# Kernel tuning notes

Measured on AMD Instinct MI355X. Metric: run time of the kernel, lower is better.

Reference implementation:

```python
import jax, jax.numpy as jnp
import numpy as np
from jax import lax

NSITE, NCELL, BSZ = 101, 64, 1
D_MODEL, D_INNER, D_STATE, D_CONV, DT_RANK = 64, 128, 16, 4, 4
L = NSITE * NCELL


def setup_inputs() -> dict:
    key = jax.random.key(0)
    ks = jax.random.split(key, 16)
    f = lambda k, s, sc=0.05: jax.random.normal(k, s, jnp.float32) * sc
    return {
        "DNAinput": f(ks[0], (BSZ, L, 32), 1.0),
        "CpGinput": f(ks[1], (BSZ, L, 16), 1.0),
        "cellinput": f(ks[2], (BSZ, L, 16), 1.0),
        "pos": f(ks[3], (BSZ, L, D_MODEL), 1.0),
        "y_true": jax.random.uniform(ks[4], (64,), jnp.float32),
        "W_fcc": f(ks[5], (64, D_MODEL)),
        "b_fcc": jnp.zeros((D_MODEL,), jnp.float32),
        "W_in": f(ks[6], (D_MODEL, 2 * D_INNER)),
        "conv_w": f(ks[7], (D_INNER, D_CONV)),
        "conv_b": jnp.zeros((D_INNER,), jnp.float32),
        "W_xp": f(ks[8], (D_INNER, DT_RANK + 2 * D_STATE)),
        "W_dt": f(ks[9], (DT_RANK, D_INNER)),
        "b_dt": f(ks[10], (D_INNER,)),
        "A_log": jnp.log(jnp.broadcast_to(jnp.arange(1, D_STATE + 1, dtype=jnp.float32), (D_INNER, D_STATE))),
        "Dres": jnp.ones((D_INNER,), jnp.float32),
        "W_out": f(ks[11], (D_INNER, D_MODEL)),
        "ln_g": jnp.ones((D_MODEL,), jnp.float32),
        "ln_b": jnp.zeros((D_MODEL,), jnp.float32),
        "W_fc": f(ks[12], (D_MODEL, 1)),
        "b_fc": jnp.zeros((1,), jnp.float32),
        "halfwin": 50,
        "row_index_s": jax.random.randint(ks[13], (64,), 0, NCELL),
    }


def _silu(x):
    return x * jax.nn.sigmoid(x)


def _layernorm(x, g, b, eps=1e-5):
    m = jnp.mean(x, -1, keepdims=True)
    v = jnp.var(x, -1, keepdims=True)
    return (x - m) * lax.rsqrt(v + eps) * g + b


def _mamba(x, W_in, conv_w, conv_b, W_xp, W_dt, b_dt, A_log, Dres, W_out):
    # x: (B, L, d_model)
    xz = x @ W_in                                   # (B, L, 2*d_inner)
    xi, z = jnp.split(xz, 2, axis=-1)
    # depthwise causal conv1d, kernel D_CONV
    xt = xi.transpose(0, 2, 1)                      # (B, d_inner, L)
    xc = lax.conv_general_dilated(
        xt, conv_w[:, None, :], (1,), [(D_CONV - 1, 0)],
        feature_group_count=D_INNER, dimension_numbers=("NCH", "OIH", "NCH"))
    xc = _silu((xc + conv_b[None, :, None]).transpose(0, 2, 1))  # (B, L, d_inner)
    xdbl = xc @ W_xp                                # (B, L, dt_rank + 2*d_state)
    dt = jax.nn.softplus(xdbl[..., :DT_RANK] @ W_dt + b_dt)      # (B, L, d_inner)
    Bm = xdbl[..., DT_RANK:DT_RANK + D_STATE]       # (B, L, d_state)
    Cm = xdbl[..., DT_RANK + D_STATE:]              # (B, L, d_state)
    A = -jnp.exp(A_log)                             # (d_inner, d_state)
    a_bar = jnp.exp(dt[..., None] * A)              # (B, L, d_inner, d_state)
    b_bar = (dt * xc)[..., None] * Bm[..., None, :]

    def comb(e1, e2):
        a1, b1 = e1
        a2, b2 = e2
        return a1 * a2, a2 * b1 + b2

    _, h = lax.associative_scan(comb, (a_bar, b_bar), axis=1)    # h_t = a_t h_{t-1} + b_t
    y = jnp.einsum("blds,bls->bld", h, Cm) + xc * Dres
    return (y * _silu(z)) @ W_out


def reference(DNAinput, CpGinput, cellinput, pos, y_true, W_fcc, b_fcc, W_in, conv_w, conv_b, W_xp, W_dt, b_dt, A_log, Dres, W_out, ln_g, ln_b, W_fc, b_fc, halfwin, row_index_s):
    x = jnp.concatenate((CpGinput, cellinput, DNAinput), -1) + pos
    x = (x @ W_fcc + b_fcc).reshape(BSZ, -1, D_MODEL)
    mb = lambda u: _mamba(u, W_in, conv_w, conv_b, W_xp, W_dt, b_dt, A_log, Dres, W_out)
    for _ in range(4):
        x = _layernorm(x + (mb(x) + jnp.flip(mb(jnp.flip(x, 1)), 1)) / 2, ln_g, ln_b)
        x = x.reshape(BSZ, NSITE, NCELL, D_MODEL).transpose(0, 2, 1, 3).reshape(BSZ, -1, D_MODEL)
        x = _layernorm(x + (mb(x) + jnp.flip(mb(jnp.flip(x, 1)), 1)) / 2, ln_g, ln_b)
        x = x.reshape(BSZ, NCELL, NSITE, D_MODEL).transpose(0, 2, 1, 3).reshape(BSZ, -1, D_MODEL)
    y_hat = (x.reshape(BSZ, NSITE, NCELL, D_MODEL) @ W_fc + b_fc)[..., 0]  # (B, nsite, ncell)
    y_sel = y_hat[0, halfwin, row_index_s].reshape(-1)
    return 1.0 - jnp.abs(y_true - jax.nn.sigmoid(y_sel))
```

## Files before the change

### kernel.cpp

```cpp
#include <hip/hip_runtime.h>
#include <math.h>

#define L_SEQ 6464
#define DM 64
#define DI 128
#define DS 16
#define CHUNK 101
#define NCH 64

__global__ void k_embed(const float* __restrict__ DNA, const float* __restrict__ CpG,
                        const float* __restrict__ cell, const float* __restrict__ pos,
                        const float* __restrict__ Wfcc, const float* __restrict__ bfcc,
                        float* __restrict__ x0) {
    int l = blockIdx.x;
    int j = threadIdx.x;
    __shared__ float in64[64];
    float v;
    if (j < 16)       v = CpG[l * 16 + j];
    else if (j < 32)  v = cell[l * 16 + (j - 16)];
    else              v = DNA[l * 32 + (j - 32)];
    v += pos[l * 64 + j];
    in64[j] = v;
    __syncthreads();
    float acc = bfcc[j];
    for (int i = 0; i < 64; i++) acc += in64[i] * Wfcc[i * 64 + j];
    x0[(size_t)l * 64 + j] = acc;
}

__global__ void __launch_bounds__(256) k_gemm_in(const float* __restrict__ x,
                                                 const float* __restrict__ Win,
                                                 float* __restrict__ xz) {
    __shared__ float s_x[8][64];
    int t0 = blockIdx.x * 8;
    int tid = threadIdx.x;
    for (int i = tid; i < 8 * 64; i += 256) {
        int rr = i >> 6, c = i & 63;
        s_x[rr][c] = x[(size_t)(t0 + rr) * 64 + c];
    }
    __syncthreads();
    int j = tid;
    float acc[8];
    #pragma unroll
    for (int r = 0; r < 8; r++) acc[r] = 0.f;
    for (int i = 0; i < 64; i++) {
        float w = Win[i * 256 + j];
        #pragma unroll
        for (int r = 0; r < 8; r++) acc[r] = fmaf(s_x[r][i], w, acc[r]);
    }
    #pragma unroll
    for (int r = 0; r < 8; r++) xz[(size_t)(t0 + r) * 256 + j] = acc[r];
}

__global__ void __launch_bounds__(256) k_convdt(
        const float* __restrict__ xz, const float* __restrict__ convw,
        const float* __restrict__ convb, const float* __restrict__ Wxp,
        const float* __restrict__ Wdt, const float* __restrict__ bdt,
        float* __restrict__ xc, float* __restrict__ dt, float* __restrict__ BC) {
    __shared__ __align__(16) float s_xi[22][128];
    __shared__ __align__(16) float s_xc[16][128];
    __shared__ float s_xd[16][36];
    __shared__ __align__(16) float s_wxpT[36][132];
    int t0 = blockIdx.x * 16;
    int tid = threadIdx.x;
    for (int i = tid; i < 36 * 128; i += 256) {
        int ii = i / 36, t = i - ii * 36;
        s_wxpT[t][ii] = Wxp[i];
    }
    for (int i = tid; i < 22 * 32; i += 256) {
        int rr = i >> 5, q = i & 31;
        int r = t0 - 3 + rr;
        float4 v = make_float4(0.f, 0.f, 0.f, 0.f);
        if (r >= 0 && r < L_SEQ) v = *(const float4*)&xz[(size_t)r * 256 + 4 * q];
        s_xi[rr][4 * q + 0] = v.x;
        s_xi[rr][4 * q + 1] = v.y;
        s_xi[rr][4 * q + 2] = v.z;
        s_xi[rr][4 * q + 3] = v.w;
    }
    __syncthreads();
    for (int dir = 0; dir < 2; dir++) {
        for (int i = tid; i < 16 * 128; i += 256) {
            int rr = i >> 7, d = i & 127;
            int lr = rr + 3;
            float acc = convb[d];
            if (dir == 0) {
                #pragma unroll
                for (int k = 0; k < 4; k++) acc += convw[d * 4 + k] * s_xi[lr - 3 + k][d];
            } else {
                #pragma unroll
                for (int k = 0; k < 4; k++) acc += convw[d * 4 + k] * s_xi[lr + 3 - k][d];
            }
            float v = acc / (1.f + expf(-acc));
            s_xc[rr][d] = v;
            xc[((size_t)dir * L_SEQ + t0 + rr) * 128 + d] = v;
        }
        __syncthreads();
        for (int o = tid; o < 16 * 36; o += 256) {
            int rr = o / 36, t = o % 36;
            float acc = 0.f;
            #pragma unroll 8
            for (int i = 0; i < 128; i += 4) {
                const float4 xv = *(const float4*)&s_xc[rr][i];
                const float4 wv = *(const float4*)&s_wxpT[t][i];
                acc = fmaf(xv.x, wv.x, acc);
                acc = fmaf(xv.y, wv.y, acc);
                acc = fmaf(xv.z, wv.z, acc);
                acc = fmaf(xv.w, wv.w, acc);
            }
            s_xd[rr][t] = acc;
        }
        __syncthreads();
        for (int o = tid; o < 16 * 128; o += 256) {
            int rr = o >> 7, d = o & 127;
            float pre = bdt[d];
            #pragma unroll
            for (int r = 0; r < 4; r++) pre += s_xd[rr][r] * Wdt[r * 128 + d];
            float dtv = (pre > 20.f) ? pre : log1pf(expf(pre));
            dt[((size_t)dir * L_SEQ + t0 + rr) * 128 + d] = dtv;
        }
        for (int o = tid; o < 16 * 32; o += 256) {
            int rr = o >> 5, w = o & 31;
            BC[((size_t)dir * L_SEQ + t0 + rr) * 32 + w] = s_xd[rr][4 + w];
        }
        __syncthreads();
    }
}

__global__ void __launch_bounds__(256) k_scanA(
        const float* __restrict__ dt, const float* __restrict__ xc,
        const float* __restrict__ BC, const float* __restrict__ Alog,
        float* __restrict__ cA, float* __restrict__ cB) {
    __shared__ __align__(16) float s_dt[CHUNK * 32];
    __shared__ __align__(16) float s_xc[CHUNK * 32];
    __shared__ __align__(16) float s_b [CHUNK * 16];
    int g    = blockIdx.x;
    int c    = blockIdx.y;
    int dir  = blockIdx.z;
    int tid  = threadIdx.x;
    int dl = tid >> 3, sp = tid & 7;
    int d = g * 32 + dl;
    const float* dtp = dt + (size_t)dir * L_SEQ * DI;
    const float* xcp = xc + (size_t)dir * L_SEQ * DI;
    const float* bcp = BC + (size_t)dir * L_SEQ * 32;
    int t0 = c * CHUNK;
    int slab0 = dir ? (L_SEQ - CHUNK - t0) : t0;
    for (int i = tid; i < CHUNK * 8; i += 256) {
        int ro = i >> 3, q = i & 7;
        int row = slab0 + ro;
        int tl = dir ? (CHUNK - 1 - ro) : ro;
        *(float4*)&s_dt[tl * 32 + 4 * q] = *(const float4*)&dtp[(size_t)row * DI + g * 32 + 4 * q];
        *(float4*)&s_xc[tl * 32 + 4 * q] = *(const float4*)&xcp[(size_t)row * DI + g * 32 + 4 * q];
    }
    for (int i = tid; i < CHUNK * 4; i += 256) {
        int ro = i >> 2, q = i & 3;
        int row = slab0 + ro;
        int tl = dir ? (CHUNK - 1 - ro) : ro;
        *(float4*)&s_b[tl * 16 + 4 * q] = *(const float4*)&bcp[(size_t)row * 32 + 4 * q];
    }
    float A0 = -expf(Alog[d * 16 + 2 * sp]);
    float A1 = -expf(Alog[d * 16 + 2 * sp + 1]);
    __syncthreads();
    float h0 = 0.f, h1 = 0.f, ap0 = 1.f, ap1 = 1.f;
    #pragma unroll 4
    for (int tl = 0; tl < CHUNK; tl++) {
        float dv = s_dt[tl * 32 + dl];
        float xv = s_xc[tl * 32 + dl];
        float t1 = dv * xv;
        float2 bq = *(const float2*)&s_b[tl * 16 + 2 * sp];
        float a0 = __expf(dv * A0); h0 = fmaf(a0, h0, t1 * bq.x); ap0 *= a0;
        float a1 = __expf(dv * A1); h1 = fmaf(a1, h1, t1 * bq.y); ap1 *= a1;
    }
    size_t o0 = (size_t)dir * 131072 + (size_t)c * 2048 + (size_t)(2 * sp) * 128 + d;
    size_t o1 = o0 + 128;
    cA[o0] = ap0; cB[o0] = h0;
    cA[o1] = ap1; cB[o1] = h1;
}

__global__ void __launch_bounds__(256) k_fold(const float* __restrict__ cA,
                                              const float* __restrict__ cB,
                                              float* __restrict__ F) {
    int idx = blockIdx.x * 256 + threadIdx.x;
    int dir = idx >> 11;
    int rem = idx & 2047;
    int s = rem >> 7;
    int d = rem & 127;
    size_t o = (size_t)dir * 131072 + (size_t)s * 128 + d;
    float carry = 0.f;
    for (int cc = 0; cc < NCH; cc += 8) {
        float av[8], bv[8];
        #pragma unroll
        for (int j = 0; j < 8; j++) {
            size_t oo = o + (size_t)(cc + j) * 2048;
            av[j] = cA[oo];
            bv[j] = cB[oo];
        }
        #pragma unroll
        for (int j = 0; j < 8; j++) {
            F[o + (size_t)(cc + j) * 2048] = carry;
            carry = fmaf(av[j], carry, bv[j]);
        }
    }
}

__global__ void __launch_bounds__(256) k_scanB(
        const float* __restrict__ dt, const float* __restrict__ xc,
        const float* __restrict__ BC, const float* __restrict__ Alog,
        const float* __restrict__ Dres, const float* __restrict__ F,
        float* __restrict__ y) {
    __shared__ __align__(16) float s_dt[CHUNK * 32];
    __shared__ __align__(16) float s_xc[CHUNK * 32];
    __shared__ __align__(16) float s_bc[CHUNK * 32];
    int g    = blockIdx.x;
    int c    = blockIdx.y;
    int dir  = blockIdx.z;
    int tid  = threadIdx.x;
    int dl = tid >> 3, sp = tid & 7;
    int d = g * 32 + dl;
    const float* dtp = dt + (size_t)dir * L_SEQ * DI;
    const float* xcp = xc + (size_t)dir * L_SEQ * DI;
    const float* bcp = BC + (size_t)dir * L_SEQ * 32;
    float* yp = y + (size_t)dir * L_SEQ * DI;
    int t0 = c * CHUNK;
    int slab0 = dir ? (L_SEQ - CHUNK - t0) : t0;
    for (int i = tid; i < CHUNK * 8; i += 256) {
        int ro = i >> 3, q = i & 7;
        int row = slab0 + ro;
        int tl = dir ? (CHUNK - 1 - ro) : ro;
        *(float4*)&s_dt[tl * 32 + 4 * q] = *(const float4*)&dtp[(size_t)row * DI + g * 32 + 4 * q];
        *(float4*)&s_xc[tl * 32 + 4 * q] = *(const float4*)&xcp[(size_t)row * DI + g * 32 + 4 * q];
        *(float4*)&s_bc[tl * 32 + 4 * q] = *(const float4*)&bcp[(size_t)row * 32 + 4 * q];
    }
    float A0 = -expf(Alog[d * 16 + 2 * sp]);
    float A1 = -expf(Alog[d * 16 + 2 * sp + 1]);
    size_t o0 = (size_t)dir * 131072 + (size_t)c * 2048 + (size_t)(2 * sp) * 128 + d;
    float h0 = F[o0];
    float h1 = F[o0 + 128];
    float Dv = Dres[d];
    __syncthreads();
    #pragma unroll 4
    for (int tl = 0; tl < CHUNK; tl++) {
        float dv = s_dt[tl * 32 + dl];
        float xv = s_xc[tl * 32 + dl];
        float t1 = dv * xv;
        float2 bq = *(const float2*)&s_bc[tl * 32 + 2 * sp];
        float2 cq = *(const float2*)&s_bc[tl * 32 + 16 + 2 * sp];
        float a0 = __expf(dv * A0); h0 = fmaf(a0, h0, t1 * bq.x);
        float a1 = __expf(dv * A1); h1 = fmaf(a1, h1, t1 * bq.y);
        float p0 = h0 * cq.x, p1 = h1 * cq.y;
        float qv = p0 + p1;
        float rv = qv + __shfl_xor(qv, 1);
        float uv = rv + __shfl_xor(rv, 2);
        float val = uv + __shfl_xor(uv, 4);
        if (sp == 0) s_dt[tl * 32 + dl] = val + xv * Dv;
    }
    __syncthreads();
    for (int i = tid; i < CHUNK * 8; i += 256) {
        int ro = i >> 3, q = i & 7;
        int row = slab0 + ro;
        int tl = dir ? (CHUNK - 1 - ro) : ro;
        float4 v = *(const float4*)&s_dt[tl * 32 + 4 * q];
        *(float4*)&yp[(size_t)row * DI + g * 32 + 4 * q] = v;
    }
}

__global__ void __launch_bounds__(256) k_outln(
        const float* __restrict__ x, const float* __restrict__ y,
        const float* __restrict__ xz, const float* __restrict__ Wout,
        const float* __restrict__ Win, const float* __restrict__ lng,
        const float* __restrict__ lnb, float* __restrict__ xnext,
        float* __restrict__ xznext, int permMode, int doXz) {
    __shared__ float s_g[4][128];
    __shared__ float s_out[4][64];
    __shared__ int s_l2[4];
    int tid = threadIdx.x;
    int w = tid >> 6;
    int j = tid & 63;
    int l = blockIdx.x * 4 + w;
    float z1 = xz[(size_t)l * 256 + 128 + j];
    float z2 = xz[(size_t)l * 256 + 192 + j];
    float sz1 = z1 / (1.f + expf(-z1));
    float sz2 = z2 / (1.f + expf(-z2));
    s_g[w][j]      = 0.5f * (y[(size_t)l * 128 + j] + y[(size_t)(L_SEQ + l) * 128 + j]) * sz1;
    s_g[w][j + 64] = 0.5f * (y[(size_t)l * 128 + 64 + j] + y[(size_t)(L_SEQ + l) * 128 + 64 + j]) * sz2;
    __syncthreads();
    float acc = x[(size_t)l * 64 + j];
    for (int i = 0; i < 128; i++) acc += s_g[w][i] * Wout[i * 64 + j];
    float m = acc;
    for (int o = 32; o >= 1; o >>= 1) m += __shfl_xor(m, o);
    m *= (1.f / 64.f);
    float dv = acc - m;
    float v = dv * dv;
    for (int o = 32; o >= 1; o >>= 1) v += __shfl_xor(v, o);
    v *= (1.f / 64.f);
    float out = dv * rsqrtf(v + 1e-5f) * lng[j] + lnb[j];
    int l2;
    if (permMode == 0) l2 = (l % 64) * 101 + (l / 64);
    else               l2 = (l % 101) * 64 + (l / 101);
    xnext[(size_t)l2 * 64 + j] = out;
    if (!doXz) return;
    s_out[w][j] = out;
    if (j == 0) s_l2[w] = l2;
    __syncthreads();
    float xa[4];
    #pragma unroll
    for (int r = 0; r < 4; r++) xa[r] = 0.f;
    for (int i = 0; i < 64; i++) {
        float wv = Win[i * 256 + tid];
        #pragma unroll
        for (int r = 0; r < 4; r++) xa[r] = fmaf(s_out[r][i], wv, xa[r]);
    }
    #pragma unroll
    for (int r = 0; r < 4; r++) xznext[(size_t)s_l2[r] * 256 + tid] = xa[r];
}

__global__ void k_epilogue(const float* __restrict__ x, const float* __restrict__ Wfc,
                           const float* __restrict__ bfc, const float* __restrict__ ytrue,
                           const int* __restrict__ halfwin, const int* __restrict__ rows,
                           float* __restrict__ out) {
    int k = threadIdx.x;
    int hw = halfwin[0];
    int c = rows[k];
    const float* xr = x + ((size_t)hw * 64 + c) * 64;
    float acc = bfc[0];
    for (int i = 0; i < 64; i++) acc += xr[i] * Wfc[i];
    float s = 1.f / (1.f + expf(-acc));
    float r = 1.f - fabsf(ytrue[k] - s);
    out[k] = r;
}

extern "C" void kernel_launch(void* const* d_in, const int* in_sizes, int n_in,
                              void* d_out, int out_size, void* d_ws, size_t ws_size,
                              hipStream_t stream) {
    const float* DNA   = (const float*)d_in[0];
    const float* CpG   = (const float*)d_in[1];
    const float* cel   = (const float*)d_in[2];
    const float* pos   = (const float*)d_in[3];
    const float* ytrue = (const float*)d_in[4];
    const float* Wfcc  = (const float*)d_in[5];
    const float* bfcc  = (const float*)d_in[6];
    const float* Win   = (const float*)d_in[7];
    const float* convw = (const float*)d_in[8];
    const float* convb = (const float*)d_in[9];
    const float* Wxp   = (const float*)d_in[10];
    const float* Wdt   = (const float*)d_in[11];
    const float* bdt   = (const float*)d_in[12];
    const float* Alog  = (const float*)d_in[13];
    const float* Dres  = (const float*)d_in[14];
    const float* Wout  = (const float*)d_in[15];
    const float* lng   = (const float*)d_in[16];
    const float* lnb   = (const float*)d_in[17];
    const float* Wfc   = (const float*)d_in[18];
    const float* bfc   = (const float*)d_in[19];
    const int* halfwin = (const int*)d_in[20];
    const int* rows    = (const int*)d_in[21];

    float* ws = (float*)d_ws;
    size_t off = 0;
    float* x0  = ws + off; off += (size_t)L_SEQ * 64;
    float* x1  = ws + off; off += (size_t)L_SEQ * 64;
    float* xzA = ws + off; off += (size_t)L_SEQ * 256;
    float* xzB = ws + off; off += (size_t)L_SEQ * 256;
    float* xcb = ws + off; off += (size_t)2 * L_SEQ * 128;
    float* dtb = ws + off; off += (size_t)2 * L_SEQ * 128;
    float* BCb = ws + off; off += (size_t)2 * L_SEQ * 32;
    float* yb  = ws + off; off += (size_t)2 * L_SEQ * 128;
    float* cAb = ws + off; off += (size_t)2 * NCH * 2048;
    float* cBb = ws + off; off += (size_t)2 * NCH * 2048;
    float* Fb  = ws + off; off += (size_t)2 * NCH * 2048;

    k_embed<<<L_SEQ, 64, 0, stream>>>(DNA, CpG, cel, pos, Wfcc, bfcc, x0);

    float* xcur = x0;
    float* xnxt = x1;
    float* xzc  = xzA;
    float* xzn  = xzB;
    k_gemm_in<<<L_SEQ / 8, 256, 0, stream>>>(xcur, Win, xzc);
    for (int sb = 0; sb < 8; sb++) {
        k_convdt<<<L_SEQ / 16, 256, 0, stream>>>(xzc, convw, convb, Wxp, Wdt, bdt, xcb, dtb, BCb);
        k_scanA<<<dim3(4, NCH, 2), 256, 0, stream>>>(dtb, xcb, BCb, Alog, cAb, cBb);
        k_fold<<<16, 256, 0, stream>>>(cAb, cBb, Fb);
        k_scanB<<<dim3(4, NCH, 2), 256, 0, stream>>>(dtb, xcb, BCb, Alog, Dres, Fb, yb);
        k_outln<<<L_SEQ / 4, 256, 0, stream>>>(xcur, yb, xzc, Wout, Win, lng, lnb, xnxt, xzn,
                                               (sb % 2 == 0) ? 0 : 1, (sb < 7) ? 1 : 0);
        float* tmp = xcur; xcur = xnxt; xnxt = tmp;
        float* tz = xzc; xzc = xzn; xzn = tz;
    }

    k_epilogue<<<1, 64, 0, stream>>>(xcur, Wfc, bfc, ytrue, halfwin, rows, (float*)d_out);
}
```

Before: 736.2 us.

## Shorten scan chunks, split convdt by direction, fuse embed into input GEMM

The chunked selective scan now uses 202 chunks of 32 steps instead of 64 chunks of 101, so the scan kernels launch many more blocks and each runs a shorter serial loop. The sequential carry fold grows to 202 steps. The conv/dt kernel gets a second grid dimension for direction, doubling its blocks at the cost of loading the xz tile and transposed weights twice. The embedding kernel is merged into the first input projection to save one launch and one global round trip.

```diff
diff --git a/kernel.cpp b/kernel.cpp
--- a/kernel.cpp
+++ b/kernel.cpp
@@ -5,37 +5,36 @@
 #define DM 64
 #define DI 128
 #define DS 16
-#define CHUNK 101
-#define NCH 64
-
-__global__ void k_embed(const float* __restrict__ DNA, const float* __restrict__ CpG,
-                        const float* __restrict__ cell, const float* __restrict__ pos,
-                        const float* __restrict__ Wfcc, const float* __restrict__ bfcc,
-                        float* __restrict__ x0) {
-    int l = blockIdx.x;
-    int j = threadIdx.x;
-    __shared__ float in64[64];
-    float v;
-    if (j < 16)       v = CpG[l * 16 + j];
-    else if (j < 32)  v = cell[l * 16 + (j - 16)];
-    else              v = DNA[l * 32 + (j - 32)];
-    v += pos[l * 64 + j];
-    in64[j] = v;
-    __syncthreads();
-    float acc = bfcc[j];
-    for (int i = 0; i < 64; i++) acc += in64[i] * Wfcc[i * 64 + j];
-    x0[(size_t)l * 64 + j] = acc;
-}
-
-__global__ void __launch_bounds__(256) k_gemm_in(const float* __restrict__ x,
-                                                 const float* __restrict__ Win,
-                                                 float* __restrict__ xz) {
+#define CLEN 32
+#define NCHK 202
+#define CTOT (NCHK * 2048)
+
+__global__ void __launch_bounds__(256) k_front0(
+        const float* __restrict__ DNA, const float* __restrict__ CpG,
+        const float* __restrict__ cell, const float* __restrict__ pos,
+        const float* __restrict__ Wfcc, const float* __restrict__ bfcc,
+        const float* __restrict__ Win, float* __restrict__ x0,
+        float* __restrict__ xz) {
+    __shared__ float s_in[8][64];
     __shared__ float s_x[8][64];
     int t0 = blockIdx.x * 8;
     int tid = threadIdx.x;
-    for (int i = tid; i < 8 * 64; i += 256) {
-        int rr = i >> 6, c = i & 63;
-        s_x[rr][c] = x[(size_t)(t0 + rr) * 64 + c];
+    for (int e = tid; e < 8 * 64; e += 256) {
+        int r = e >> 6, j = e & 63;
+        int l = t0 + r;
+        float v;
+        if (j < 16)       v = CpG[l * 16 + j];
+        else if (j < 32)  v = cell[l * 16 + (j - 16)];
+        else              v = DNA[l * 32 + (j - 32)];
+        s_in[r][j] = v + pos[l * 64 + j];
+    }
+    __syncthreads();
+    for (int e = tid; e < 8 * 64; e += 256) {
+        int r = e >> 6, j = e & 63;
+        float acc = bfcc[j];
+        for (int i = 0; i < 64; i++) acc += s_in[r][i] * Wfcc[i * 64 + j];
+        s_x[r][j] = acc;
+        x0[(size_t)(t0 + r) * 64 + j] = acc;
     }
     __syncthreads();
     int j = tid;
@@ -61,6 +60,7 @@
     __shared__ float s_xd[16][36];
     __shared__ __align__(16) float s_wxpT[36][132];
     int t0 = blockIdx.x * 16;
+    int dir = blockIdx.y;
     int tid = threadIdx.x;
     for (int i = tid; i < 36 * 128; i += 256) {
         int ii = i / 36, t = i - ii * 36;
@@ -77,51 +77,48 @@
         s_xi[rr][4 * q + 3] = v.w;
     }
     __syncthreads();
-    for (int dir = 0; dir < 2; dir++) {
-        for (int i = tid; i < 16 * 128; i += 256) {
-            int rr = i >> 7, d = i & 127;
-            int lr = rr + 3;
-            float acc = convb[d];
-            if (dir == 0) {
-                #pragma unroll
-                for (int k = 0; k < 4; k++) acc += convw[d * 4 + k] * s_xi[lr - 3 + k][d];
-            } else {
-                #pragma unroll
-                for (int k = 0; k < 4; k++) acc += convw[d * 4 + k] * s_xi[lr + 3 - k][d];
-            }
-            float v = acc / (1.f + expf(-acc));
-            s_xc[rr][d] = v;
-            xc[((size_t)dir * L_SEQ + t0 + rr) * 128 + d] = v;
+    for (int i = tid; i < 16 * 128; i += 256) {
+        int rr = i >> 7, d = i & 127;
+        int lr = rr + 3;
+        float acc = convb[d];
+        if (dir == 0) {
+            #pragma unroll
+            for (int k = 0; k < 4; k++) acc += convw[d * 4 + k] * s_xi[lr - 3 + k][d];
+        } else {
+            #pragma unroll
+            for (int k = 0; k < 4; k++) acc += convw[d * 4 + k] * s_xi[lr + 3 - k][d];
         }
-        __syncthreads();
-        for (int o = tid; o < 16 * 36; o += 256) {
-            int rr = o / 36, t = o % 36;
-            float acc = 0.f;
-            #pragma unroll 8
-            for (int i = 0; i < 128; i += 4) {
-                const float4 xv = *(const float4*)&s_xc[rr][i];
-                const float4 wv = *(const float4*)&s_wxpT[t][i];
-                acc = fmaf(xv.x, wv.x, acc);
-                acc = fmaf(xv.y, wv.y, acc);
-                acc = fmaf(xv.z, wv.z, acc);
-                acc = fmaf(xv.w, wv.w, acc);
-            }
-            s_xd[rr][t] = acc;
+        float v = acc / (1.f + expf(-acc));
+        s_xc[rr][d] = v;
+        xc[((size_t)dir * L_SEQ + t0 + rr) * 128 + d] = v;
+    }
+    __syncthreads();
+    for (int o = tid; o < 16 * 36; o += 256) {
+        int rr = o / 36, t = o % 36;
+        float acc = 0.f;
+        #pragma unroll 8
+        for (int i = 0; i < 128; i += 4) {
+            const float4 xv = *(const float4*)&s_xc[rr][i];
+            const float4 wv = *(const float4*)&s_wxpT[t][i];
+            acc = fmaf(xv.x, wv.x, acc);
+            acc = fmaf(xv.y, wv.y, acc);
+            acc = fmaf(xv.z, wv.z, acc);
+            acc = fmaf(xv.w, wv.w, acc);
         }
-        __syncthreads();
-        for (int o = tid; o < 16 * 128; o += 256) {
-            int rr = o >> 7, d = o & 127;
-            float pre = bdt[d];
-            #pragma unroll
-            for (int r = 0; r < 4; r++) pre += s_xd[rr][r] * Wdt[r * 128 + d];
-            float dtv = (pre > 20.f) ? pre : log1pf(expf(pre));
-            dt[((size_t)dir * L_SEQ + t0 + rr) * 128 + d] = dtv;
-        }
-        for (int o = tid; o < 16 * 32; o += 256) {
-            int rr = o >> 5, w = o & 31;
-            BC[((size_t)dir * L_SEQ + t0 + rr) * 32 + w] = s_xd[rr][4 + w];
-        }
-        __syncthreads();
+        s_xd[rr][t] = acc;
+    }
+    __syncthreads();
+    for (int o = tid; o < 16 * 128; o += 256) {
+        int rr = o >> 7, d = o & 127;
+        float pre = bdt[d];
+        #pragma unroll
+        for (int r = 0; r < 4; r++) pre += s_xd[rr][r] * Wdt[r * 128 + d];
+        float dtv = (pre > 20.f) ? pre : log1pf(expf(pre));
+        dt[((size_t)dir * L_SEQ + t0 + rr) * 128 + d] = dtv;
+    }
+    for (int o = tid; o < 16 * 32; o += 256) {
+        int rr = o >> 5, w = o & 31;
+        BC[((size_t)dir * L_SEQ + t0 + rr) * 32 + w] = s_xd[rr][4 + w];
     }
 }
 
@@ -129,9 +126,9 @@
         const float* __restrict__ dt, const float* __restrict__ xc,
         const float* __restrict__ BC, const float* __restrict__ Alog,
         float* __restrict__ cA, float* __restrict__ cB) {
-    __shared__ __align__(16) float s_dt[CHUNK * 32];
-    __shared__ __align__(16) float s_xc[CHUNK * 32];
-    __shared__ __align__(16) float s_b [CHUNK * 16];
+    __shared__ __align__(16) float s_dt[CLEN * 32];
+    __shared__ __align__(16) float s_xc[CLEN * 32];
+    __shared__ __align__(16) float s_b [CLEN * 16];
     int g    = blockIdx.x;
     int c    = blockIdx.y;
     int dir  = blockIdx.z;
@@ -141,19 +138,19 @@
     const float* dtp = dt + (size_t)dir * L_SEQ * DI;
     const float* xcp = xc + (size_t)dir * L_SEQ * DI;
     const float* bcp = BC + (size_t)dir * L_SEQ * 32;
-    int t0 = c * CHUNK;
-    int slab0 = dir ? (L_SEQ - CHUNK - t0) : t0;
-    for (int i = tid; i < CHUNK * 8; i += 256) {
-        int ro = i >> 3, q = i & 7;
+    int t0 = c * CLEN;
+    int slab0 = dir ? (L_SEQ - CLEN - t0) : t0;
+    {
+        int ro = tid >> 3, q = tid & 7;
         int row = slab0 + ro;
-        int tl = dir ? (CHUNK - 1 - ro) : ro;
+        int tl = dir ? (CLEN - 1 - ro) : ro;
         *(float4*)&s_dt[tl * 32 + 4 * q] = *(const float4*)&dtp[(size_t)row * DI + g * 32 + 4 * q];
         *(float4*)&s_xc[tl * 32 + 4 * q] = *(const float4*)&xcp[(size_t)row * DI + g * 32 + 4 * q];
     }
-    for (int i = tid; i < CHUNK * 4; i += 256) {
-        int ro = i >> 2, q = i & 3;
+    if (tid < CLEN * 4) {
+        int ro = tid >> 2, q = tid & 3;
         int row = slab0 + ro;
-        int tl = dir ? (CHUNK - 1 - ro) : ro;
+        int tl = dir ? (CLEN - 1 - ro) : ro;
         *(float4*)&s_b[tl * 16 + 4 * q] = *(const float4*)&bcp[(size_t)row * 32 + 4 * q];
     }
     float A0 = -expf(Alog[d * 16 + 2 * sp]);
@@ -161,7 +158,7 @@
     __syncthreads();
     float h0 = 0.f, h1 = 0.f, ap0 = 1.f, ap1 = 1.f;
     #pragma unroll 4
-    for (int tl = 0; tl < CHUNK; tl++) {
+    for (int tl = 0; tl < CLEN; tl++) {
         float dv = s_dt[tl * 32 + dl];
         float xv = s_xc[tl * 32 + dl];
         float t1 = dv * xv;
@@ -169,10 +166,9 @@
         float a0 = __expf(dv * A0); h0 = fmaf(a0, h0, t1 * bq.x); ap0 *= a0;
         float a1 = __expf(dv * A1); h1 = fmaf(a1, h1, t1 * bq.y); ap1 *= a1;
     }
-    size_t o0 = (size_t)dir * 131072 + (size_t)c * 2048 + (size_t)(2 * sp) * 128 + d;
-    size_t o1 = o0 + 128;
+    size_t o0 = (size_t)dir * CTOT + (size_t)c * 2048 + (size_t)(2 * sp) * 128 + d;
     cA[o0] = ap0; cB[o0] = h0;
-    cA[o1] = ap1; cB[o1] = h1;
+    cA[o0 + 128] = ap1; cB[o0 + 128] = h1;
 }
 
 __global__ void __launch_bounds__(256) k_fold(const float* __restrict__ cA,
@@ -183,21 +179,22 @@
     int rem = idx & 2047;
     int s = rem >> 7;
     int d = rem & 127;
-    size_t o = (size_t)dir * 131072 + (size_t)s * 128 + d;
+    size_t o = (size_t)dir * CTOT + (size_t)s * 128 + d;
     float carry = 0.f;
-    for (int cc = 0; cc < NCH; cc += 8) {
+    int cc = 0;
+    while (cc < NCHK) {
+        int n = (NCHK - cc < 8) ? (NCHK - cc) : 8;
         float av[8], bv[8];
-        #pragma unroll
-        for (int j = 0; j < 8; j++) {
+        for (int j = 0; j < n; j++) {
             size_t oo = o + (size_t)(cc + j) * 2048;
             av[j] = cA[oo];
             bv[j] = cB[oo];
         }
-        #pragma unroll
-        for (int j = 0; j < 8; j++) {
+        for (int j = 0; j < n; j++) {
             F[o + (size_t)(cc + j) * 2048] = carry;
             carry = fmaf(av[j], carry, bv[j]);
         }
+        cc += n;
     }
 }
 
@@ -206,9 +203,9 @@
         const float* __restrict__ BC, const float* __restrict__ Alog,
         const float* __restrict__ Dres, const float* __restrict__ F,
         float* __restrict__ y) {
-    __shared__ __align__(16) float s_dt[CHUNK * 32];
-    __shared__ __align__(16) float s_xc[CHUNK * 32];
-    __shared__ __align__(16) float s_bc[CHUNK * 32];
+    __shared__ __align__(16) float s_dt[CLEN * 32];
+    __shared__ __align__(16) float s_xc[CLEN * 32];
+    __shared__ __align__(16) float s_bc[CLEN * 32];
     int g    = blockIdx.x;
     int c    = blockIdx.y;
     int dir  = blockIdx.z;
@@ -219,25 +216,25 @@
     const float* xcp = xc + (size_t)dir * L_SEQ * DI;
     const float* bcp = BC + (size_t)dir * L_SEQ * 32;
     float* yp = y + (size_t)dir * L_SEQ * DI;
-    int t0 = c * CHUNK;
-    int slab0 = dir ? (L_SEQ - CHUNK - t0) : t0;
-    for (int i = tid; i < CHUNK * 8; i += 256) {
-        int ro = i >> 3, q = i & 7;
+    int t0 = c * CLEN;
+    int slab0 = dir ? (L_SEQ - CLEN - t0) : t0;
+    {
+        int ro = tid >> 3, q = tid & 7;
         int row = slab0 + ro;
-        int tl = dir ? (CHUNK - 1 - ro) : ro;
+        int tl = dir ? (CLEN - 1 - ro) : ro;
         *(float4*)&s_dt[tl * 32 + 4 * q] = *(const float4*)&dtp[(size_t)row * DI + g * 32 + 4 * q];
         *(float4*)&s_xc[tl * 32 + 4 * q] = *(const float4*)&xcp[(size_t)row * DI + g * 32 + 4 * q];
         *(float4*)&s_bc[tl * 32 + 4 * q] = *(const float4*)&bcp[(size_t)row * 32 + 4 * q];
     }
     float A0 = -expf(Alog[d * 16 + 2 * sp]);
     float A1 = -expf(Alog[d * 16 + 2 * sp + 1]);
-    size_t o0 = (size_t)dir * 131072 + (size_t)c * 2048 + (size_t)(2 * sp) * 128 + d;
+    size_t o0 = (size_t)dir * CTOT + (size_t)c * 2048 + (size_t)(2 * sp) * 128 + d;
     float h0 = F[o0];
     float h1 = F[o0 + 128];
     float Dv = Dres[d];
     __syncthreads();
     #pragma unroll 4
-    for (int tl = 0; tl < CHUNK; tl++) {
+    for (int tl = 0; tl < CLEN; tl++) {
         float dv = s_dt[tl * 32 + dl];
         float xv = s_xc[tl * 32 + dl];
         float t1 = dv * xv;
@@ -253,10 +250,10 @@
         if (sp == 0) s_dt[tl * 32 + dl] = val + xv * Dv;
     }
     __syncthreads();
-    for (int i = tid; i < CHUNK * 8; i += 256) {
-        int ro = i >> 3, q = i & 7;
+    {
+        int ro = tid >> 3, q = tid & 7;
         int row = slab0 + ro;
-        int tl = dir ? (CHUNK - 1 - ro) : ro;
+        int tl = dir ? (CLEN - 1 - ro) : ro;
         float4 v = *(const float4*)&s_dt[tl * 32 + 4 * q];
         *(float4*)&yp[(size_t)row * DI + g * 32 + 4 * q] = v;
     }
@@ -363,22 +360,21 @@
     float* dtb = ws + off; off += (size_t)2 * L_SEQ * 128;
     float* BCb = ws + off; off += (size_t)2 * L_SEQ * 32;
     float* yb  = ws + off; off += (size_t)2 * L_SEQ * 128;
-    float* cAb = ws + off; off += (size_t)2 * NCH * 2048;
-    float* cBb = ws + off; off += (size_t)2 * NCH * 2048;
-    float* Fb  = ws + off; off += (size_t)2 * NCH * 2048;
-
-    k_embed<<<L_SEQ, 64, 0, stream>>>(DNA, CpG, cel, pos, Wfcc, bfcc, x0);
+    float* cAb = ws + off; off += (size_t)2 * CTOT;
+    float* cBb = ws + off; off += (size_t)2 * CTOT;
+    float* Fb  = ws + off; off += (size_t)2 * CTOT;
 
     float* xcur = x0;
     float* xnxt = x1;
     float* xzc  = xzA;
     float* xzn  = xzB;
-    k_gemm_in<<<L_SEQ / 8, 256, 0, stream>>>(xcur, Win, xzc);
+    k_front0<<<L_SEQ / 8, 256, 0, stream>>>(DNA, CpG, cel, pos, Wfcc, bfcc, Win, x0, xzc);
     for (int sb = 0; sb < 8; sb++) {
-        k_convdt<<<L_SEQ / 16, 256, 0, stream>>>(xzc, convw, convb, Wxp, Wdt, bdt, xcb, dtb, BCb);
-        k_scanA<<<dim3(4, NCH, 2), 256, 0, stream>>>(dtb, xcb, BCb, Alog, cAb, cBb);
+        k_convdt<<<dim3(L_SEQ / 16, 2), 256, 0, stream>>>(xzc, convw, convb, Wxp, Wdt, bdt,
+                                                          xcb, dtb, BCb);
+        k_scanA<<<dim3(4, NCHK, 2), 256, 0, stream>>>(dtb, xcb, BCb, Alog, cAb, cBb);
         k_fold<<<16, 256, 0, stream>>>(cAb, cBb, Fb);
-        k_scanB<<<dim3(4, NCH, 2), 256, 0, stream>>>(dtb, xcb, BCb, Alog, Dres, Fb, yb);
+        k_scanB<<<dim3(4, NCHK, 2), 256, 0, stream>>>(dtb, xcb, BCb, Alog, Dres, Fb, yb);
         k_outln<<<L_SEQ / 4, 256, 0, stream>>>(xcur, yb, xzc, Wout, Win, lng, lnb, xnxt, xzn,
                                                (sb % 2 == 0) ? 0 : 1, (sb < 7) ? 1 : 0);
         float* tmp = xcur; xcur = xnxt; xnxt = tmp;
```

After: 1.258 ms. 70.9% more time.
